# Optimization experiments

Measured on AMD Instinct MI355X. Metric: run time of the kernel, lower is better.

## Reference

```python
import jax, jax.numpy as jnp
import numpy as np
from jax import lax

NUM_IM, ROIS = 32, 128          # images per batch, proposals per image
NUM_CLASSES, EMBED, OBJ_DIM = 151, 200, 2048
HALF_H = 256                    # per-direction LSTM hidden; bi concat -> 512
BN_EPS = 1e-5


def _lstm_dir(xs, wih, whh, b):
    # xs: [T, B, Din] -> hidden states [T, B, H]
    pre = jnp.einsum('tbd,dh->tbh', xs, wih) + b  # precompute input proj
    H = whh.shape[0]
    h0 = jnp.zeros((xs.shape[1], H), xs.dtype)
    def step(carry, pt):
        h, c = carry
        g = pt + h @ whh
        i, f, gg, o = jnp.split(g, 4, axis=-1)
        c = jax.nn.sigmoid(f) * c + jax.nn.sigmoid(i) * jnp.tanh(gg)
        h = jax.nn.sigmoid(o) * jnp.tanh(c)
        return (h, c), h
    _, hs = lax.scan(step, (h0, h0), pre)
    return hs


def _bilstm(x, wih, whh, b):
    # x: [B, T, D] -> [B, T, 2*HALF_H]; wih/whh/b carry both directions on axis 0
    xs = jnp.swapaxes(x, 0, 1)
    fwd = _lstm_dir(xs, wih[0], whh[0], b[0])
    bwd = _lstm_dir(xs[::-1], wih[1], whh[1], b[1])[::-1]
    return jnp.swapaxes(jnp.concatenate([fwd, bwd], -1), 0, 1)


def _context(feats, conf, params):
    # sort_rois: per-image descending confidence order, run 2-layer bi(tree)LSTM,
    # then scatter back with the inverse permutation (as in _sort_by_score).
    D = feats.shape[-1]
    f = feats.reshape(NUM_IM, ROIS, D)
    perm = jnp.argsort(-conf.reshape(NUM_IM, ROIS), axis=1)
    xs = jnp.take_along_axis(f, perm[..., None], axis=1)
    wih0, whh0, b0, wih1, whh1, b1 = params
    h = _bilstm(xs, wih0, whh0, b0)
    h = _bilstm(h, wih1, whh1, b1)
    inv = jnp.argsort(perm, axis=1)
    h = jnp.take_along_axis(h, inv[..., None], axis=1)
    return h.reshape(NUM_IM * ROIS, -1)


def setup_inputs() -> dict:
    key = jax.random.key(0)
    ks = jax.random.split(key, 24)
    N = NUM_IM * ROIS
    obj_fmaps = jax.random.normal(ks[0], (N, OBJ_DIM), jnp.float32)
    obj_logits = jax.random.normal(ks[1], (N, NUM_CLASSES), jnp.float32)
    xy = jax.random.uniform(ks[2], (N, 2), jnp.float32) * 500.0
    wh = jax.random.uniform(ks[3], (N, 2), jnp.float32) * 100.0 + 1.0
    boxes = jnp.concatenate([xy, xy + wh], axis=1)  # valid x1y1x2y2
    im_inds = jnp.repeat(jnp.arange(NUM_IM, dtype=jnp.int64), ROIS)
    w = lambda k, s: (jax.random.normal(k, s, jnp.float32) * 0.02)
    H4 = 4 * HALF_H
    D_obj, D_edge = OBJ_DIM + EMBED + 128, EMBED + 2 * HALF_H + OBJ_DIM
    return {
        'obj_fmaps': obj_fmaps, 'obj_logits': obj_logits, 'boxes': boxes,
        'im_inds': im_inds,
        'obj_embed_w': w(ks[4], (NUM_CLASSES, EMBED)),
        'obj_embed2_w': w(ks[5], (NUM_CLASSES, EMBED)),
        'bn_gamma': jnp.ones((4,), jnp.float32), 'bn_beta': jnp.zeros((4,), jnp.float32),
        'bn_mean': jnp.zeros((4,), jnp.float32), 'bn_var': jnp.ones((4,), jnp.float32),
        'pos_w': w(ks[6], (4, 128)), 'pos_b': jnp.zeros((128,), jnp.float32),
        'obj_wih0': w(ks[7], (2, D_obj, H4)), 'obj_whh0': w(ks[8], (2, HALF_H, H4)),
        'obj_b0': jnp.zeros((2, H4), jnp.float32),
        'obj_wih1': w(ks[9], (2, 2 * HALF_H, H4)), 'obj_whh1': w(ks[10], (2, HALF_H, H4)),
        'obj_b1': jnp.zeros((2, H4), jnp.float32),
        'edge_wih0': w(ks[11], (2, D_edge, H4)), 'edge_whh0': w(ks[12], (2, HALF_H, H4)),
        'edge_b0': jnp.zeros((2, H4), jnp.float32),
        'edge_wih1': w(ks[13], (2, 2 * HALF_H, H4)), 'edge_whh1': w(ks[14], (2, HALF_H, H4)),
        'edge_b1': jnp.zeros((2, H4), jnp.float32),
        'dec_w': w(ks[15], (D_obj + 2 * HALF_H, NUM_CLASSES)),
        'dec_b': jnp.zeros((NUM_CLASSES,), jnp.float32),
    }


def reference(obj_fmaps, obj_logits, boxes, im_inds, obj_embed_w, obj_embed2_w,
              bn_gamma, bn_beta, bn_mean, bn_var, pos_w, pos_b,
              obj_wih0, obj_whh0, obj_b0, obj_wih1, obj_whh1, obj_b1,
              edge_wih0, edge_whh0, edge_b0, edge_wih1, edge_whh1, edge_b1,
              dec_w, dec_b):
    probs = jax.nn.softmax(obj_logits, axis=-1)
    obj_embed = probs @ obj_embed_w                      # soft class embedding
    x1, y1, x2, y2 = boxes[:, 0], boxes[:, 1], boxes[:, 2], boxes[:, 3]
    cs = jnp.stack([(x1 + x2) * 0.5, (y1 + y2) * 0.5, x2 - x1, y2 - y1], axis=-1)
    csn = (cs - bn_mean) * lax.rsqrt(bn_var + BN_EPS) * bn_gamma + bn_beta
    pos = jax.nn.relu(csn @ pos_w + pos_b)               # BN(4)+Linear(4,128)+ReLU
    feats = jnp.concatenate([obj_fmaps, obj_embed, pos], axis=-1)  # [N, 2376]
    conf = jnp.max(probs[:, 1:], axis=-1)                # confidence (non-bg)
    enc = _context(feats, conf, (obj_wih0, obj_whh0, obj_b0,
                                 obj_wih1, obj_whh1, obj_b1))       # [N, 512]
    dec_in = jnp.concatenate([feats, enc], axis=-1)      # pass_in_obj_feats_to_decoder
    obj_dists = dec_in @ dec_w + dec_b                   # [N, 151]
    obj_preds = jnp.argmax(obj_dists[:, 1:], axis=-1) + 1
    edge_in = jnp.concatenate([obj_embed2_w[obj_preds], enc, obj_fmaps], axis=-1)
    edge_ctx = _context(edge_in, conf, (edge_wih0, edge_whh0, edge_b0,
                                        edge_wih1, edge_whh1, edge_b1))  # [N, 512]
    return jnp.concatenate([obj_dists, edge_ctx], axis=-1)  # [N, 663]
```

## Files before the change

kernel.cpp:

```cpp
#include <hip/hip_runtime.h>
#include <hip/hip_bf16.h>
#include <hip/hip_fp16.h>

typedef unsigned short u16;
typedef unsigned char u8;
typedef unsigned int u32;
typedef short s16x8 __attribute__((ext_vector_type(8)));
typedef float f32x4 __attribute__((ext_vector_type(4)));
typedef int i32x4 __attribute__((ext_vector_type(4)));

#define FE_LD 2944
#define EDGE_LD 2816

static __device__ __forceinline__ int sdot4(u32 a, u32 b, int acc) {
  return __builtin_amdgcn_sdot4((int)a, (int)b, acc, false);
}
static __device__ __forceinline__ float fsig(float x) {
  return __builtin_amdgcn_rcpf(1.f + __expf(-x));
}
static __device__ __forceinline__ float ftanh(float x) {
  return 1.f - 2.f * __builtin_amdgcn_rcpf(1.f + __expf(2.f * x));
}
static __device__ __forceinline__ u16 f2bf_raw(float f) {
  return __builtin_bit_cast(u16, __float2bfloat16(f));
}

#define GLD_LDS16(gsrc, ldst) \
  __builtin_amdgcn_global_load_lds((const __attribute__((address_space(1))) void*)(gsrc), \
                                   (__attribute__((address_space(3))) void*)(ldst), 16, 0, 0)

static __device__ __forceinline__ void xcd_map(int gy, int* bx, int* by) {
  int lin = blockIdx.x;
  int q = gridDim.x >> 3;
  int wg = (lin & 7) * q + (lin >> 3);
  *bx = wg / gy; *by = wg % gy;
}

__global__ __launch_bounds__(256) void gemm_kernel(
    const u16* __restrict__ A, int lda,
    const u16* __restrict__ B, int ldb,
    int K, int N, int gy,
    float* __restrict__ outF, __hip_bfloat16* __restrict__ outB, int ldc,
    const float* __restrict__ bias)
{
  __shared__ __align__(16) u16 As[128*64];
  __shared__ __align__(16) u16 Bs[128*64];
  const int tid = threadIdx.x;
  const int w = tid >> 6, lane = tid & 63;
  const int wm = w >> 1, wn = w & 1;
  int bxi, byi; xcd_map(gy, &bxi, &byi);
  const long bm = (long)bxi * 128;
  const long bn = (long)byi * 128;
  f32x4 acc[4][4] = {};

  for (int k0 = 0; k0 < K; k0 += 64) {
    #pragma unroll
    for (int rr = 0; rr < 4; rr++) {
      int idx = rr * 256 + tid;
      int row = idx >> 3;
      int g   = idx & 7;
      int gs  = g ^ (row & 7);
      int ldst = (rr * 256 + (w << 6)) * 8;
      GLD_LDS16(A + (bm + row) * (long)lda + k0 + gs * 8, &As[ldst]);
      GLD_LDS16(B + (bn + row) * (long)ldb + k0 + gs * 8, &Bs[ldst]);
    }
    __syncthreads();
    #pragma unroll
    for (int kk = 0; kk < 2; kk++) {
      s16x8 af[4], bfr[4];
      #pragma unroll
      for (int i = 0; i < 4; i++) {
        int ra = wm * 64 + i * 16 + (lane & 15);
        int rb = wn * 64 + i * 16 + (lane & 15);
        int gg = kk * 4 + (lane >> 4);
        af[i]  = *(const s16x8*)&As[ra * 64 + ((gg ^ (ra & 7)) << 3)];
        bfr[i] = *(const s16x8*)&Bs[rb * 64 + ((gg ^ (rb & 7)) << 3)];
      }
      #pragma unroll
      for (int i = 0; i < 4; i++)
        #pragma unroll
        for (int j = 0; j < 4; j++)
          acc[i][j] = __builtin_amdgcn_mfma_f32_16x16x32_bf16(af[i], bfr[j], acc[i][j], 0, 0, 0);
    }
    __syncthreads();
  }

  #pragma unroll
  for (int i = 0; i < 4; i++)
    #pragma unroll
    for (int j = 0; j < 4; j++)
      #pragma unroll
      for (int v = 0; v < 4; v++) {
        long rr = bm + wm * 64 + i * 16 + (lane >> 4) * 4 + v;
        int  cc = (int)bn + wn * 64 + j * 16 + (lane & 15);
        if (cc < N) {
          float val = acc[i][j][v] + (bias ? bias[cc] : 0.f);
          if (outF) outF[rr * (long)ldc + cc] = val;
          else      outB[rr * (long)ldc + cc] = __float2bfloat16(val);
        }
      }
}

__global__ __launch_bounds__(256) void gemm_i8_kernel(
    const u8* __restrict__ A, int lda,
    const u8* __restrict__ B, int ldb,
    int K, int N, int gy,
    const float* __restrict__ asc, const float* __restrict__ bsc,
    __hip_bfloat16* __restrict__ outB, int ldc,
    const float* __restrict__ bias)
{
  __shared__ __align__(16) u8 As[128*128];
  __shared__ __align__(16) u8 Bs[128*128];
  const int tid = threadIdx.x;
  const int w = tid >> 6, lane = tid & 63;
  const int wm = w >> 1, wn = w & 1;
  int bxi, byi; xcd_map(gy, &bxi, &byi);
  const long bm = (long)bxi * 128;
  const long bn = (long)byi * 128;
  i32x4 acc[4][4] = {};

  for (int k0 = 0; k0 < K; k0 += 128) {
    #pragma unroll
    for (int rr = 0; rr < 4; rr++) {
      int idx = rr * 256 + tid;
      int row = idx >> 3;
      int g   = idx & 7;
      int gs  = g ^ (row & 7);
      int ldst = (rr * 256 + (w << 6)) * 16;
      GLD_LDS16(A + (bm + row) * (long)lda + k0 + gs * 16, &As[ldst]);
      GLD_LDS16(B + (bn + row) * (long)ldb + k0 + gs * 16, &Bs[ldst]);
    }
    __syncthreads();
    #pragma unroll
    for (int kk = 0; kk < 2; kk++) {
      i32x4 af[4], bfr[4];
      #pragma unroll
      for (int i = 0; i < 4; i++) {
        int ra = wm * 64 + i * 16 + (lane & 15);
        int rb = wn * 64 + i * 16 + (lane & 15);
        int gg = kk * 4 + (lane >> 4);
        af[i]  = __builtin_bit_cast(i32x4, *(const uint4*)&As[ra * 128 + ((gg ^ (ra & 7)) << 4)]);
        bfr[i] = __builtin_bit_cast(i32x4, *(const uint4*)&Bs[rb * 128 + ((gg ^ (rb & 7)) << 4)]);
      }
      #pragma unroll
      for (int i = 0; i < 4; i++)
        #pragma unroll
        for (int j = 0; j < 4; j++)
          acc[i][j] = __builtin_amdgcn_mfma_i32_16x16x64_i8(af[i], bfr[j], acc[i][j], 0, 0, 0);
    }
    __syncthreads();
  }

  #pragma unroll
  for (int i = 0; i < 4; i++)
    #pragma unroll
    for (int j = 0; j < 4; j++)
      #pragma unroll
      for (int v = 0; v < 4; v++) {
        long rr = bm + wm * 64 + i * 16 + (lane >> 4) * 4 + v;
        int  cc = (int)bn + wn * 64 + j * 16 + (lane & 15);
        if (cc < N) {
          float val = (float)acc[i][j][v] * asc[rr] * bsc[cc] + (bias ? bias[cc] : 0.f);
          outB[rr * (long)ldc + cc] = __float2bfloat16(val);
        }
      }
}

#define N_TROPS 9
struct SetupOps {
  const float* src[N_TROPS];
  __hip_bfloat16* dst[N_TROPS];
  int srcK[N_TROPS], srcN[N_TROPS], dstR[N_TROPS], dstC[N_TROPS];
  int split[N_TROPS], soff[N_TROPS];
  int tileBase[N_TROPS], tilesX[N_TROPS];
  int trEnd, pkEnd;
  const float* whh[4];
  u32* wreg[4]; u32* wlds[4]; float* wsc[4];
  const float* logits; const float* fmaps; const float* boxes;
  const float* bn_g; const float* bn_b; const float* bn_m; const float* bn_v;
  const float* pos_w; const float* pos_b; const float* embw;
  __hip_bfloat16* FE; u8* FEq; float* ascFE; float* conf;
};
__global__ __launch_bounds__(256) void setup_kernel(SetupOps ops)
{
  __shared__ __align__(16) float stage[2432];
  __shared__ float red[256];
  __shared__ float pf[151];
  const int bid = blockIdx.x, t = threadIdx.x;

  if (bid < ops.trEnd) {
    __shared__ float tile[64][65];
    int op = 0;
    #pragma unroll
    for (int i = 1; i < N_TROPS; i++) if (bid >= ops.tileBase[i]) op = i;
    const int local = bid - ops.tileBase[op];
    const int kt = (local % ops.tilesX[op]) * 64;
    const int nt = (local / ops.tilesX[op]) * 64;
    const float* src = ops.src[op];
    __hip_bfloat16* dst = ops.dst[op];
    const int srcK = ops.srcK[op], srcN = ops.srcN[op];
    const int dstR = ops.dstR[op], dstC = ops.dstC[op];
    const int split = ops.split[op], soff = ops.soff[op];
    {
      const int tx = t & 63, ty = t >> 6;
      #pragma unroll
      for (int i0 = 0; i0 < 16; i0++) {
        int i = i0 * 4 + ty;
        int k = kt + i;
        int srck = (k < split) ? (soff + k) : (k - split);
        int n = nt + tx;
        tile[i][tx] = (srck < srcK && n < srcN) ? src[(size_t)srck * srcN + n] : 0.f;
      }
    }
    __syncthreads();
    {
      const int cx = t & 31, iy = t >> 5;
      #pragma unroll
      for (int i0 = 0; i0 < 8; i0++) {
        int i = i0 * 8 + iy;
        int n = nt + i, k = kt + 2 * cx;
        if (n < dstR && k < dstC) {
          ushort2 h;
          h.x = f2bf_raw(tile[2 * cx][i]);
          h.y = f2bf_raw(tile[2 * cx + 1][i]);
          *(ushort2*)&dst[(size_t)n * dstC + k] = h;
        }
      }
    }
    return;
  }

  if (bid < ops.pkEnd) {
    const int local = bid - ops.trEnd;
    const int set = local >> 3;
    const int idx = (local & 7) * 256 + t;
    const float* whh = ops.whh[set];
    u32* wreg = ops.wreg[set];
    u32* wlds = ops.wlds[set];
    float* wsc = ops.wsc[set];
    const int d = idx >> 10, col = idx & 1023;
    const int c4 = col >> 8, j = col & 255;
    const float* s = whh + (size_t)d * 256 * 1024 + col;
    float mx = 0.f;
    for (int k = 0; k < 256; k++) mx = fmaxf(mx, fabsf(s[(size_t)k * 1024]));
    float inv = (mx > 0.f) ? 127.f / mx : 0.f;
    wsc[d * 1024 + col] = (mx > 0.f) ? mx / (127.f * 127.f) : 0.f;
    const int rc = (c4 < 2) ? 12 : 8;
    const int rb = (c4 == 0) ? 0 : (c4 == 1) ? 12 : (c4 == 2) ? 24 : 32;
    for (int kg = 0; kg < 4; kg++) {
      const int slot = kg * 256 + j;
      for (int w = 0; w < 16; w++) {
        u32 v = 0;
        #pragma unroll
        for (int b = 0; b < 4; b++) {
          int q = __float2int_rn(s[(size_t)(kg * 64 + 4 * w + b) * 1024] * inv);
          q = max(-127, min(127, q));
          v |= ((u32)(q & 0xff)) << (8 * b);
        }
        if (w < rc) {
          wreg[(size_t)(d * 40 + rb + w) * 1024 + slot] = v;
        } else {
          int qq, comp;
          if (c4 == 0)      { qq = 0; comp = w - 12; }
          else if (c4 == 1) { qq = 1; comp = w - 12; }
          else if (c4 == 2) { qq = 2 + ((w - 8) >> 2); comp = (w - 8) & 3; }
          else              { qq = 4 + ((w - 8) >> 2); comp = (w - 8) & 3; }
          wlds[((size_t)(d * 6 + qq) * 1024 + slot) * 4 + comp] = v;
        }
      }
    }
    return;
  }

  const int row = bid - ops.pkEnd;
  float v = (t < 151) ? ops.logits[(size_t)row * 151 + t] : -3.0e38f;
  red[t] = v; __syncthreads();
  for (int s = 128; s > 0; s >>= 1) { if (t < s) red[t] = fmaxf(red[t], red[t + s]); __syncthreads(); }
  float mx = red[0]; __syncthreads();
  float p = (t < 151) ? expf(v - mx) : 0.f;
  red[t] = p; __syncthreads();
  for (int s = 128; s > 0; s >>= 1) { if (t < s) red[t] += red[t + s]; __syncthreads(); }
  float sum = red[0]; __syncthreads();
  p = p / sum;
  if (t < 151) pf[t] = p;
  red[t] = (t >= 1 && t < 151) ? p : 0.f; __syncthreads();
  for (int s = 128; s > 0; s >>= 1) { if (t < s) red[t] = fmaxf(red[t], red[t + s]); __syncthreads(); }
  if (t == 0) ops.conf[row] = red[0];
  __syncthreads();

  __hip_bfloat16* FE = ops.FE + (size_t)row * FE_LD;
  {
    const float4* fm4 = (const float4*)(ops.fmaps + (size_t)row * 2048);
    for (int q4 = t; q4 < 512; q4 += 256) {
      float4 f = fm4[q4];
      *(float4*)&stage[q4 * 4] = f;
      ushort4 h;
      h.x = f2bf_raw(f.x); h.y = f2bf_raw(f.y); h.z = f2bf_raw(f.z); h.w = f2bf_raw(f.w);
      *(ushort4*)&FE[512 + q4 * 4] = h;
    }
  }
  if (t < 50) {
    const float4* ew4 = (const float4*)(ops.embw);
    float4 e = {0.f, 0.f, 0.f, 0.f};
    for (int k = 0; k < 151; k++) {
      float4 w = ew4[k * 50 + t];
      float pk = pf[k];
      e.x += pk * w.x; e.y += pk * w.y; e.z += pk * w.z; e.w += pk * w.w;
    }
    *(float4*)&stage[2048 + 4 * t] = e;
    ushort4 h;
    h.x = f2bf_raw(e.x); h.y = f2bf_raw(e.y); h.z = f2bf_raw(e.z); h.w = f2bf_raw(e.w);
    *(ushort4*)&FE[2560 + 4 * t] = h;
  }
  if (t < 128) {
    float x1 = ops.boxes[row * 4 + 0], y1 = ops.boxes[row * 4 + 1];
    float x2 = ops.boxes[row * 4 + 2], y2 = ops.boxes[row * 4 + 3];
    float cs[4] = { (x1 + x2) * 0.5f, (y1 + y2) * 0.5f, x2 - x1, y2 - y1 };
    float a = ops.pos_b[t];
    #pragma unroll
    for (int j = 0; j < 4; j++) {
      float cn = (cs[j] - ops.bn_m[j]) * rsqrtf(ops.bn_v[j] + 1e-5f) * ops.bn_g[j] + ops.bn_b[j];
      a += cn * ops.pos_w[j * 128 + t];
    }
    a = fmaxf(a, 0.f);
    stage[2248 + t] = a;
    FE[2760 + t] = __float2bfloat16(a);
  }
  if (t < 56) { stage[2376 + t] = 0.f; FE[2888 + t] = __float2bfloat16(0.f); }
  __syncthreads();

  float qm = 0.f;
  for (int c = t; c < 2432; c += 256) qm = fmaxf(qm, fabsf(stage[c]));
  red[t] = qm; __syncthreads();
  for (int s = 128; s > 0; s >>= 1) { if (t < s) red[t] = fmaxf(red[t], red[t + s]); __syncthreads(); }
  qm = red[0];
  float inv = (qm > 0.f) ? 127.f / qm : 0.f;
  if (t == 0) ops.ascFE[row] = (qm > 0.f) ? qm / 127.f : 0.f;
  u32* d32 = (u32*)(ops.FEq + (size_t)row * 2432);
  for (int wd = t; wd < 608; wd += 256) {
    u32 vv = 0;
    #pragma unroll
    for (int b = 0; b < 4; b++) {
      int q = __float2int_rn(stage[4 * wd + b] * inv);
      q = max(-127, min(127, q));
      vv |= ((u32)(q & 0xff)) << (8 * b);
    }
    d32[wd] = vv;
  }
}

__global__ __launch_bounds__(256) void quantw_sort_kernel(
    const u16* __restrict__ w0, u8* __restrict__ w0q, float* __restrict__ bsc0,
    const u16* __restrict__ w1, u8* __restrict__ w1q, float* __restrict__ bsc1,
    const float* __restrict__ conf, int* __restrict__ perm)
{
  const int bid = blockIdx.x, t = threadIdx.x;
  if (bid < 4096) {
    __shared__ float red[256];
    const int row = (bid < 2048) ? bid : (bid - 2048);
    const u16* src = (bid < 2048) ? w0 : w1;
    u8* dst = (bid < 2048) ? w0q : w1q;
    float* sc = (bid < 2048) ? bsc0 : bsc1;
    const int K = (bid < 2048) ? 2432 : 2816;
    const uint4* s4 = (const uint4*)(src + (size_t)row * K);
    const int K8 = K >> 3;
    float mx = 0.f;
    for (int c8 = t; c8 < K8; c8 += 256) {
      uint4 v = s4[c8];
      #pragma unroll
      for (int wi = 0; wi < 4; wi++) {
        u32 w = (wi == 0) ? v.x : (wi == 1) ? v.y : (wi == 2) ? v.z : v.w;
        mx = fmaxf(mx, fabsf(__builtin_bit_cast(float, w << 16)));
        mx = fmaxf(mx, fabsf(__builtin_bit_cast(float, w & 0xffff0000u)));
      }
    }
    red[t] = mx; __syncthreads();
    for (int st = 128; st > 0; st >>= 1) { if (t < st) red[t] = fmaxf(red[t], red[t + st]); __syncthreads(); }
    mx = red[0];
    float inv = (mx > 0.f) ? 127.f / mx : 0.f;
    if (t == 0) sc[row] = (mx > 0.f) ? mx / 127.f : 0.f;
    uint2* d64 = (uint2*)(dst + (size_t)row * K);
    for (int c8 = t; c8 < K8; c8 += 256) {
      uint4 v = s4[c8];
      u32 out[2] = {0, 0};
      #pragma unroll
      for (int wi = 0; wi < 4; wi++) {
        u32 w = (wi == 0) ? v.x : (wi == 1) ? v.y : (wi == 2) ? v.z : v.w;
        float f0 = __builtin_bit_cast(float, w << 16);
        float f1 = __builtin_bit_cast(float, w & 0xffff0000u);
        int q0 = max(-127, min(127, __float2int_rn(f0 * inv)));
        int q1 = max(-127, min(127, __float2int_rn(f1 * inv)));
        out[wi >> 1] |= ((u32)(q0 & 0xff)) << (16 * (wi & 1));
        out[wi >> 1] |= ((u32)(q1 & 0xff)) << (16 * (wi & 1) + 8);
      }
      d64[c8] = uint2{out[0], out[1]};
    }
    return;
  }
  {
    __shared__ float key[128];
    __shared__ int   idx[128];
    const int b = bid - 4096;
    if (t < 128) { key[t] = conf[b * 128 + t]; idx[t] = t; }
    __syncthreads();
    for (int k = 2; k <= 128; k <<= 1)
      for (int j = k >> 1; j > 0; j >>= 1) {
        if (t < 128) {
          int ixj = t ^ j;
          if (ixj > t) {
            bool up = (t & k) == 0;
            float ka = key[t], kb = key[ixj];
            int ia = idx[t], ib = idx[ixj];
            bool before = (ka > kb) || (ka == kb && ia < ib);
            if (before != up) { key[t] = kb; key[ixj] = ka; idx[t] = ib; idx[ixj] = ia; }
          }
        }
        __syncthreads();
      }
    if (t < 128) perm[b * 128 + t] = b * 128 + idx[t];
  }
}

__global__ __launch_bounds__(1024) void rec_kernel(
    const __hip_bfloat16* __restrict__ P,
    const int* __restrict__ perm,
    const u32* __restrict__ wreg_g,
    const uint4* __restrict__ wlds_g,
    const float* __restrict__ wsc_g,
    int gatherPerm, int outPerm,
    __hip_bfloat16* __restrict__ out_bf, int out_ld,
    float* __restrict__ out_f32, int f32_ld, int f32_off)
{
  __shared__ __align__(16) uint4 wt4[6 * 1024];
  __shared__ __align__(16) int4 part[256 * 5];
  __shared__ __align__(16) u32 hq[64];
  __shared__ int prow_lds[128];
  const int tid = threadIdx.x;
  const int kg = tid >> 8;
  const int img = blockIdx.x & 31, dir = blockIdx.x >> 5;

  u32 wv[40];
  {
    const u32* rp = wreg_g + (size_t)dir * 40960 + tid;
    #pragma unroll
    for (int i = 0; i < 40; i++) wv[i] = rp[(size_t)i * 1024];
  }
  #pragma unroll
  for (int i = 0; i < 40; i++) asm volatile("" : "+v"(wv[i]));
  {
    const uint4* lp = wlds_g + (size_t)dir * 6144 + tid;
    #pragma unroll
    for (int q = 0; q < 6; q++) wt4[q * 1024 + tid] = lp[(size_t)q * 1024];
  }
  if (tid < 128) prow_lds[tid] = perm[img * 128 + tid];
  if (tid < 64) hq[tid] = 0;

  float sc0 = 0.f, sc1 = 0.f, sc2 = 0.f, sc3 = 0.f, cst = 0.f;
  if (tid < 256) {
    const float* sp = wsc_g + dir * 1024 + tid;
    sc0 = sp[0]; sc1 = sp[256]; sc2 = sp[512]; sc3 = sp[768];
  }
  __syncthreads();

  const uint4* hq4 = (const uint4*)hq;

  int st = dir ? 127 : 0;
  float p0 = 0.f, p1 = 0.f, p2 = 0.f, p3 = 0.f;
  if (tid < 256) {
    int prow0 = gatherPerm ? prow_lds[st] : (img * 128 + st);
    const __hip_bfloat16* pp = P + (size_t)prow0 * 2048 + dir * 1024 + tid;
    p0 = __bfloat162float(pp[0]);   p1 = __bfloat162float(pp[256]);
    p2 = __bfloat162float(pp[512]); p3 = __bfloat162float(pp[768]);
  }

  for (int t = 0; t < 128; t++) {
    float n0 = 0.f, n1 = 0.f, n2 = 0.f, n3 = 0.f;
    if (tid < 256 && t < 127) {
      int stn = dir ? (126 - t) : (t + 1);
      int prn = gatherPerm ? prow_lds[stn] : (img * 128 + stn);
      const __hip_bfloat16* pp = P + (size_t)prn * 2048 + dir * 1024 + tid;
      n0 = __bfloat162float(pp[0]);   n1 = __bfloat162float(pp[256]);
      n2 = __bfloat162float(pp[512]); n3 = __bfloat162float(pp[768]);
    }

    int a0 = 0, a1 = 0, a2 = 0, a3 = 0;
    {
      uint4 hv = hq4[kg * 4 + 0];
      a0 = sdot4(hv.x, wv[0], a0);  a0 = sdot4(hv.y, wv[1], a0);
      a0 = sdot4(hv.z, wv[2], a0);  a0 = sdot4(hv.w, wv[3], a0);
      a1 = sdot4(hv.x, wv[12], a1); a1 = sdot4(hv.y, wv[13], a1);
      a1 = sdot4(hv.z, wv[14], a1); a1 = sdot4(hv.w, wv[15], a1);
      a2 = sdot4(hv.x, wv[24], a2); a2 = sdot4(hv.y, wv[25], a2);
      a2 = sdot4(hv.z, wv[26], a2); a2 = sdot4(hv.w, wv[27], a2);
      a3 = sdot4(hv.x, wv[32], a3); a3 = sdot4(hv.y, wv[33], a3);
      a3 = sdot4(hv.z, wv[34], a3); a3 = sdot4(hv.w, wv[35], a3);
    }
    {
      uint4 hv = hq4[kg * 4 + 1];
      a0 = sdot4(hv.x, wv[4], a0);  a0 = sdot4(hv.y, wv[5], a0);
      a0 = sdot4(hv.z, wv[6], a0);  a0 = sdot4(hv.w, wv[7], a0);
      a1 = sdot4(hv.x, wv[16], a1); a1 = sdot4(hv.y, wv[17], a1);
      a1 = sdot4(hv.z, wv[18], a1); a1 = sdot4(hv.w, wv[19], a1);
      a2 = sdot4(hv.x, wv[28], a2); a2 = sdot4(hv.y, wv[29], a2);
      a2 = sdot4(hv.z, wv[30], a2); a2 = sdot4(hv.w, wv[31], a2);
      a3 = sdot4(hv.x, wv[36], a3); a3 = sdot4(hv.y, wv[37], a3);
      a3 = sdot4(hv.z, wv[38], a3); a3 = sdot4(hv.w, wv[39], a3);
    }
    {
      uint4 hv = hq4[kg * 4 + 2];
      a0 = sdot4(hv.x, wv[8], a0);  a0 = sdot4(hv.y, wv[9], a0);
      a0 = sdot4(hv.z, wv[10], a0); a0 = sdot4(hv.w, wv[11], a0);
      a1 = sdot4(hv.x, wv[20], a1); a1 = sdot4(hv.y, wv[21], a1);
      a1 = sdot4(hv.z, wv[22], a1); a1 = sdot4(hv.w, wv[23], a1);
      uint4 wl = wt4[2 * 1024 + tid];
      a2 = sdot4(hv.x, wl.x, a2); a2 = sdot4(hv.y, wl.y, a2);
      a2 = sdot4(hv.z, wl.z, a2); a2 = sdot4(hv.w, wl.w, a2);
      wl = wt4[4 * 1024 + tid];
      a3 = sdot4(hv.x, wl.x, a3); a3 = sdot4(hv.y, wl.y, a3);
      a3 = sdot4(hv.z, wl.z, a3); a3 = sdot4(hv.w, wl.w, a3);
    }
    {
      uint4 hv = hq4[kg * 4 + 3];
      uint4 wl = wt4[0 * 1024 + tid];
      a0 = sdot4(hv.x, wl.x, a0); a0 = sdot4(hv.y, wl.y, a0);
      a0 = sdot4(hv.z, wl.z, a0); a0 = sdot4(hv.w, wl.w, a0);
      wl = wt4[1 * 1024 + tid];
      a1 = sdot4(hv.x, wl.x, a1); a1 = sdot4(hv.y, wl.y, a1);
      a1 = sdot4(hv.z, wl.z, a1); a1 = sdot4(hv.w, wl.w, a1);
      wl = wt4[3 * 1024 + tid];
      a2 = sdot4(hv.x, wl.x, a2); a2 = sdot4(hv.y, wl.y, a2);
      a2 = sdot4(hv.z, wl.z, a2); a2 = sdot4(hv.w, wl.w, a2);
      wl = wt4[5 * 1024 + tid];
      a3 = sdot4(hv.x, wl.x, a3); a3 = sdot4(hv.y, wl.y, a3);
      a3 = sdot4(hv.z, wl.z, a3); a3 = sdot4(hv.w, wl.w, a3);
    }

    part[(tid & 255) * 5 + kg] = int4{a0, a1, a2, a3};
    __syncthreads();

    if (tid < 256) {
      int4 q0 = part[tid * 5 + 0], q1 = part[tid * 5 + 1];
      int4 q2 = part[tid * 5 + 2], q3 = part[tid * 5 + 3];
      float gi = (float)(q0.x + q1.x + q2.x + q3.x) * sc0 + p0;
      float gf = (float)(q0.y + q1.y + q2.y + q3.y) * sc1 + p1;
      float gg = (float)(q0.z + q1.z + q2.z + q3.z) * sc2 + p2;
      float go = (float)(q0.w + q1.w + q2.w + q3.w) * sc3 + p3;
      float si = fsig(gi), sf = fsig(gf), so = fsig(go);
      cst = sf * cst + si * ftanh(gg);
      float h = so * ftanh(cst);
      int qi = __float2int_rn(h * 127.f);
      ((signed char*)hq)[tid] = (signed char)qi;
      const int orow = outPerm ? prow_lds[st] : (img * 128 + st);
      if (out_bf)  out_bf[(size_t)orow * out_ld + dir * 256 + tid] = __float2bfloat16(h);
      if (out_f32) out_f32[(size_t)orow * f32_ld + f32_off + dir * 256 + tid] = h;
    }
    __syncthreads();
    p0 = n0; p1 = n1; p2 = n2; p3 = n3;
    st = dir ? (st - 1) : (st + 1);
  }
}

__global__ __launch_bounds__(256) void argmax_edge_kernel(
    const float* __restrict__ dists,
    const float* __restrict__ embed2,
    const float* __restrict__ fmaps,
    const __hip_bfloat16* __restrict__ FE,
    u8* __restrict__ EDGEq, float* __restrict__ ascEDGE)
{
  __shared__ __align__(16) float stage[EDGE_LD];
  __shared__ float rv[256];
  __shared__ int   ri[256];
  const int row = blockIdx.x, t = threadIdx.x;

  float best = (t < 150) ? dists[(size_t)row * 663 + 1 + t] : -3.4e38f;
  int   bi   = (t < 150) ? (1 + t) : 1000;
  rv[t] = best; ri[t] = bi;
  __syncthreads();
  for (int s = 128; s > 0; s >>= 1) {
    if (t < s) {
      float ov = rv[t + s]; int oi = ri[t + s];
      if (ov > rv[t] || (ov == rv[t] && oi < ri[t])) { rv[t] = ov; ri[t] = oi; }
    }
    __syncthreads();
  }
  const int pr = ri[0];

  for (int c0 = t; c0 < 200; c0 += 256)
    stage[c0] = embed2[(size_t)pr * 200 + c0];
  if (t < 64) {
    const uint4* e4 = (const uint4*)(FE + (size_t)row * FE_LD);
    uint4 v = e4[t];
    #pragma unroll
    for (int wi = 0; wi < 4; wi++) {
      u32 w = (wi == 0) ? v.x : (wi == 1) ? v.y : (wi == 2) ? v.z : v.w;
      stage[200 + t * 8 + wi * 2]     = __builtin_bit_cast(float, w << 16);
      stage[200 + t * 8 + wi * 2 + 1] = __builtin_bit_cast(float, w & 0xffff0000u);
    }
  }
  {
    const float4* fm4 = (const float4*)(fmaps + (size_t)row * 2048);
    for (int c4 = t; c4 < 512; c4 += 256)
      *(float4*)&stage[712 + c4 * 4] = fm4[c4];
  }
  if (t < 56) stage[2760 + t] = 0.f;
  __syncthreads();

  float qm = 0.f;
  for (int c = t; c < EDGE_LD; c += 256) qm = fmaxf(qm, fabsf(stage[c]));
  rv[t] = qm; __syncthreads();
  for (int s = 128; s > 0; s >>= 1) { if (t < s) rv[t] = fmaxf(rv[t], rv[t + s]); __syncthreads(); }
  qm = rv[0];
  float inv = (qm > 0.f) ? 127.f / qm : 0.f;
  if (t == 0) ascEDGE[row] = (qm > 0.f) ? qm / 127.f : 0.f;
  uint2* d64 = (uint2*)(EDGEq + (size_t)row * EDGE_LD);
  for (int wd8 = t; wd8 < (EDGE_LD >> 3); wd8 += 256) {
    u32 out[2] = {0, 0};
    #pragma unroll
    for (int b = 0; b < 8; b++) {
      int q = __float2int_rn(stage[8 * wd8 + b] * inv);
      q = max(-127, min(127, q));
      out[b >> 2] |= ((u32)(q & 0xff)) << (8 * (b & 3));
    }
    d64[wd8] = uint2{out[0], out[1]};
  }
}

extern "C" void kernel_launch(void* const* d_in, const int* in_sizes, int n_in,
                              void* d_out, int out_size, void* d_ws, size_t ws_size,
                              hipStream_t stream)
{
  const float* obj_fmaps    = (const float*)d_in[0];
  const float* obj_logits   = (const float*)d_in[1];
  const float* boxes        = (const float*)d_in[2];
  const float* obj_embed_w  = (const float*)d_in[4];
  const float* obj_embed2_w = (const float*)d_in[5];
  const float* bn_g = (const float*)d_in[6];
  const float* bn_b = (const float*)d_in[7];
  const float* bn_m = (const float*)d_in[8];
  const float* bn_v = (const float*)d_in[9];
  const float* pos_w = (const float*)d_in[10];
  const float* pos_b = (const float*)d_in[11];
  const float* obj_wih0 = (const float*)d_in[12];
  const float* obj_whh0 = (const float*)d_in[13];
  const float* obj_b0   = (const float*)d_in[14];
  const float* obj_wih1 = (const float*)d_in[15];
  const float* obj_whh1 = (const float*)d_in[16];
  const float* obj_b1   = (const float*)d_in[17];
  const float* edge_wih0 = (const float*)d_in[18];
  const float* edge_whh0 = (const float*)d_in[19];
  const float* edge_b0   = (const float*)d_in[20];
  const float* edge_wih1 = (const float*)d_in[21];
  const float* edge_whh1 = (const float*)d_in[22];
  const float* edge_b1   = (const float*)d_in[23];
  const float* dec_w = (const float*)d_in[24];
  const float* dec_b = (const float*)d_in[25];
  float* out = (float*)d_out;

  char* ws = (char*)d_ws;
  auto alloc = [&](size_t bytes) -> char* {
    char* p = ws; ws += (bytes + 255) & ~(size_t)255; return p;
  };
  __hip_bfloat16* FE     = (__hip_bfloat16*)alloc(4096ull * FE_LD * 2);
  __hip_bfloat16* Pbuf   = (__hip_bfloat16*)alloc(4096ull * 2048 * 2);
  __hip_bfloat16* hseq   = (__hip_bfloat16*)alloc(4096ull * 512 * 2);
  __hip_bfloat16* wih0T  = (__hip_bfloat16*)alloc(2048ull * 2432 * 2);
  __hip_bfloat16* wih1T  = (__hip_bfloat16*)alloc(2048ull * 512 * 2);
  __hip_bfloat16* ewih0T = (__hip_bfloat16*)alloc(2048ull * 2816 * 2);
  __hip_bfloat16* ewih1T = (__hip_bfloat16*)alloc(2048ull * 512 * 2);
  __hip_bfloat16* decT   = (__hip_bfloat16*)alloc(256ull * 2944 * 2);
  u32* whh0pk  = (u32*)alloc(133120ull * 4);
  u32* whh1pk  = (u32*)alloc(133120ull * 4);
  u32* ewhh0pk = (u32*)alloc(133120ull * 4);
  u32* ewhh1pk = (u32*)alloc(133120ull * 4);
  u8*  FEq     = (u8*)alloc(4096ull * 2432);
  u8*  EDGEq   = (u8*)alloc(4096ull * 2816);
  u8*  wih0q   = (u8*)alloc(2048ull * 2432);
  u8*  ewih0q  = (u8*)alloc(2048ull * 2816);
  float* ascFE   = (float*)alloc(4096 * 4);
  float* ascEDGE = (float*)alloc(4096 * 4);
  float* bsc0    = (float*)alloc(2048 * 4);
  float* bsc1    = (float*)alloc(2048 * 4);
  int*   perm  = (int*)alloc(4096 * 4);
  float* conf  = (float*)alloc(4096 * 4);
  (void)in_sizes; (void)n_in; (void)out_size; (void)ws_size;

  SetupOps so{};
  int nt = 0, base = 0;
  auto addTr = [&](const float* src, __hip_bfloat16* dst, int srcK, int srcN,
                   int dstR, int dstC, int split, int soff) {
    so.src[nt] = src; so.dst[nt] = dst;
    so.srcK[nt] = srcK; so.srcN[nt] = srcN; so.dstR[nt] = dstR; so.dstC[nt] = dstC;
    so.split[nt] = split; so.soff[nt] = soff;
    int tx = (dstC + 63) / 64, ty = (dstR + 63) / 64;
    so.tileBase[nt] = base; so.tilesX[nt] = tx;
    base += tx * ty; nt++;
  };
  for (int d = 0; d < 2; d++) {
    addTr(obj_wih0 + (size_t)d * 2376 * 1024, wih0T + (size_t)d * 1024 * 2432, 2376, 1024, 1024, 2432, 0, 0);
    addTr(obj_wih1 + (size_t)d * 512 * 1024,  wih1T + (size_t)d * 1024 * 512,  512, 1024, 1024, 512, 0, 0);
    addTr(edge_wih0 + (size_t)d * 2760 * 1024, ewih0T + (size_t)d * 1024 * 2816, 2760, 1024, 1024, 2816, 0, 0);
    addTr(edge_wih1 + (size_t)d * 512 * 1024,  ewih1T + (size_t)d * 1024 * 512,  512, 1024, 1024, 512, 0, 0);
  }
  addTr(dec_w, decT, 2888, 151, 256, 2944, 512, 2376);
  so.trEnd = base;
  so.pkEnd = base + 32;
  const float* whhs[4] = {obj_whh0, obj_whh1, edge_whh0, edge_whh1};
  u32* pks[4] = {whh0pk, whh1pk, ewhh0pk, ewhh1pk};
  for (int i = 0; i < 4; i++) {
    so.whh[i] = whhs[i];
    so.wreg[i] = pks[i];
    so.wlds[i] = pks[i] + 81920;
    so.wsc[i]  = (float*)(pks[i] + 131072);
  }
  so.logits = obj_logits; so.fmaps = obj_fmaps; so.boxes = boxes;
  so.bn_g = bn_g; so.bn_b = bn_b; so.bn_m = bn_m; so.bn_v = bn_v;
  so.pos_w = pos_w; so.pos_b = pos_b; so.embw = obj_embed_w;
  so.FE = FE; so.FEq = FEq; so.ascFE = ascFE; so.conf = conf;
  setup_kernel<<<dim3(so.pkEnd + 4096), dim3(256), 0, stream>>>(so);

  quantw_sort_kernel<<<dim3(4128), dim3(256), 0, stream>>>(
      (const u16*)wih0T, wih0q, bsc0, (const u16*)ewih0T, ewih0q, bsc1, conf, perm);

  auto gemm = [&](const void* A, int lda, const void* B, int ldb, int K, int N,
                  float* oF, __hip_bfloat16* oB, int ldc, const float* bias) {
    int gy = (N + 127) / 128;
    gemm_kernel<<<dim3(32 * gy), dim3(256), 0, stream>>>(
        (const u16*)A, lda, (const u16*)B, ldb, K, N, gy, oF, oB, ldc, bias);
  };
  auto gemm_i8 = [&](const u8* A, int lda, const u8* B, int ldb, int K, int N,
                     const float* asc, const float* bsc,
                     __hip_bfloat16* oB, int ldc, const float* bias) {
    int gy = (N + 127) / 128;
    gemm_i8_kernel<<<dim3(32 * gy), dim3(256), 0, stream>>>(
        A, lda, B, ldb, K, N, gy, asc, bsc, oB, ldc, bias);
  };
  auto rec = [&](const __hip_bfloat16* P, const u32* wpk, int gat, int op,
                 __hip_bfloat16* ob, int old_, float* of, int fld, int foff) {
    rec_kernel<<<dim3(64), dim3(1024), 0, stream>>>(
        P, perm, wpk, (const uint4*)(wpk + 81920), (const float*)(wpk + 131072),
        gat, op, ob, old_, of, fld, foff);
  };

  gemm_i8(FEq, 2432, wih0q, 2432, 2432, 2048, ascFE, bsc0, Pbuf, 2048, obj_b0);
  rec(Pbuf, whh0pk, 1, 0, hseq, 512, nullptr, 0, 0);
  gemm(hseq, 512, wih1T, 512, 512, 2048, nullptr, Pbuf, 2048, obj_b1);
  rec(Pbuf, whh1pk, 0, 1, FE, FE_LD, nullptr, 0, 0);
  gemm(FE, FE_LD, decT, 2944, 2944, 151, out, nullptr, 663, dec_b);
  argmax_edge_kernel<<<dim3(4096), dim3(256), 0, stream>>>(
      out, obj_embed2_w, obj_fmaps, FE, EDGEq, ascEDGE);
  gemm_i8(EDGEq, 2816, ewih0q, 2816, 2816, 2048, ascEDGE, bsc1, Pbuf, 2048, edge_b0);
  rec(Pbuf, ewhh0pk, 1, 0, hseq, 512, nullptr, 0, 0);
  gemm(hseq, 512, ewih1T, 512, 512, 2048, nullptr, Pbuf, 2048, edge_b1);
  rec(Pbuf, ewhh1pk, 0, 1, nullptr, 0, out, 663, 151);
}
```

Before: 821.3 us.

## Quantize input weights directly from fp32 during transpose, skipping bf16 intermediate

The large layer-0 input-projection weights were previously transposed to bf16 and then re-read by a separate kernel that computed per-row scales and quantized them to int8. Now a first kernel computes partial per-column absolute maxima straight from the fp32 source. The transpose kernel then uses those maxima to write int8 output directly, and the bf16 intermediate buffers are dropped. This removes one full write and read of roughly 20 MB of bf16 weights, at the cost of a strided column-max pass over the fp32 weights. The scales are now derived from fp32 values rather than bf16-rounded ones, so the quantized weights can differ slightly.

```diff
diff --git a/kernel.cpp b/kernel.cpp
--- a/kernel.cpp
+++ b/kernel.cpp
@@ -166,14 +166,9 @@
       }
 }
 
-#define N_TROPS 9
-struct SetupOps {
-  const float* src[N_TROPS];
-  __hip_bfloat16* dst[N_TROPS];
-  int srcK[N_TROPS], srcN[N_TROPS], dstR[N_TROPS], dstC[N_TROPS];
-  int split[N_TROPS], soff[N_TROPS];
-  int tileBase[N_TROPS], tilesX[N_TROPS];
-  int trEnd, pkEnd;
+struct PrepA {
+  const float* objw; const float* edgew;
+  float* partial;
   const float* whh[4];
   u32* wreg[4]; u32* wlds[4]; float* wsc[4];
   const float* logits; const float* fmaps; const float* boxes;
@@ -181,57 +176,31 @@
   const float* pos_w; const float* pos_b; const float* embw;
   __hip_bfloat16* FE; u8* FEq; float* ascFE; float* conf;
 };
-__global__ __launch_bounds__(256) void setup_kernel(SetupOps ops)
+__global__ __launch_bounds__(256) void prepA_kernel(PrepA ops)
 {
   __shared__ __align__(16) float stage[2432];
   __shared__ float red[256];
   __shared__ float pf[151];
   const int bid = blockIdx.x, t = threadIdx.x;
 
-  if (bid < ops.trEnd) {
-    __shared__ float tile[64][65];
-    int op = 0;
-    #pragma unroll
-    for (int i = 1; i < N_TROPS; i++) if (bid >= ops.tileBase[i]) op = i;
-    const int local = bid - ops.tileBase[op];
-    const int kt = (local % ops.tilesX[op]) * 64;
-    const int nt = (local / ops.tilesX[op]) * 64;
-    const float* src = ops.src[op];
-    __hip_bfloat16* dst = ops.dst[op];
-    const int srcK = ops.srcK[op], srcN = ops.srcN[op];
-    const int dstR = ops.dstR[op], dstC = ops.dstC[op];
-    const int split = ops.split[op], soff = ops.soff[op];
-    {
-      const int tx = t & 63, ty = t >> 6;
-      #pragma unroll
-      for (int i0 = 0; i0 < 16; i0++) {
-        int i = i0 * 4 + ty;
-        int k = kt + i;
-        int srck = (k < split) ? (soff + k) : (k - split);
-        int n = nt + tx;
-        tile[i][tx] = (srck < srcK && n < srcN) ? src[(size_t)srck * srcN + n] : 0.f;
-      }
-    }
-    __syncthreads();
-    {
-      const int cx = t & 31, iy = t >> 5;
-      #pragma unroll
-      for (int i0 = 0; i0 < 8; i0++) {
-        int i = i0 * 8 + iy;
-        int n = nt + i, k = kt + 2 * cx;
-        if (n < dstR && k < dstC) {
-          ushort2 h;
-          h.x = f2bf_raw(tile[2 * cx][i]);
-          h.y = f2bf_raw(tile[2 * cx + 1][i]);
-          *(ushort2*)&dst[(size_t)n * dstC + k] = h;
-        }
-      }
-    }
+  if (bid < 128) {
+    const int set = bid >> 6;
+    const int b6 = bid & 63;
+    const int cb = b6 & 7, ks = b6 >> 3;
+    const int r = cb * 256 + t;
+    const int d = r >> 10, c = r & 1023;
+    const int K = set ? 2760 : 2376;
+    const int K8 = K / 8;
+    const float* src = (set ? ops.edgew : ops.objw) + (size_t)d * K * 1024 + c;
+    float m = 0.f;
+    for (int k = ks * K8; k < (ks + 1) * K8; k++)
+      m = fmaxf(m, fabsf(src[(size_t)k * 1024]));
+    ops.partial[(size_t)set * 16384 + ks * 2048 + r] = m;
     return;
   }
 
-  if (bid < ops.pkEnd) {
-    const int local = bid - ops.trEnd;
+  if (bid < 160) {
+    const int local = bid - 128;
     const int set = local >> 3;
     const int idx = (local & 7) * 256 + t;
     const float* whh = ops.whh[set];
@@ -272,7 +241,7 @@
     return;
   }
 
-  const int row = bid - ops.pkEnd;
+  const int row = bid - 160;
   float v = (t < 151) ? ops.logits[(size_t)row * 151 + t] : -3.0e38f;
   red[t] = v; __syncthreads();
   for (int s = 128; s > 0; s >>= 1) { if (t < s) red[t] = fmaxf(red[t], red[t + s]); __syncthreads(); }
@@ -349,59 +318,99 @@
   }
 }
 
-__global__ __launch_bounds__(256) void quantw_sort_kernel(
-    const u16* __restrict__ w0, u8* __restrict__ w0q, float* __restrict__ bsc0,
-    const u16* __restrict__ w1, u8* __restrict__ w1q, float* __restrict__ bsc1,
-    const float* __restrict__ conf, int* __restrict__ perm)
+#define N_OPS 9
+struct Setup2 {
+  const float* src[N_OPS];
+  void* dst[N_OPS];
+  const float* partial[N_OPS];
+  float* bscOut[N_OPS];
+  int rowBase[N_OPS];
+  int srcK[N_OPS], srcN[N_OPS], dstR[N_OPS], dstC[N_OPS];
+  int split[N_OPS], soff[N_OPS], isI8[N_OPS];
+  int tileBase[N_OPS], tilesX[N_OPS];
+  int trEnd;
+  const float* conf; int* perm;
+};
+__global__ __launch_bounds__(256) void setup2_kernel(Setup2 ops)
 {
   const int bid = blockIdx.x, t = threadIdx.x;
-  if (bid < 4096) {
-    __shared__ float red[256];
-    const int row = (bid < 2048) ? bid : (bid - 2048);
-    const u16* src = (bid < 2048) ? w0 : w1;
-    u8* dst = (bid < 2048) ? w0q : w1q;
-    float* sc = (bid < 2048) ? bsc0 : bsc1;
-    const int K = (bid < 2048) ? 2432 : 2816;
-    const uint4* s4 = (const uint4*)(src + (size_t)row * K);
-    const int K8 = K >> 3;
-    float mx = 0.f;
-    for (int c8 = t; c8 < K8; c8 += 256) {
-      uint4 v = s4[c8];
-      #pragma unroll
-      for (int wi = 0; wi < 4; wi++) {
-        u32 w = (wi == 0) ? v.x : (wi == 1) ? v.y : (wi == 2) ? v.z : v.w;
-        mx = fmaxf(mx, fabsf(__builtin_bit_cast(float, w << 16)));
-        mx = fmaxf(mx, fabsf(__builtin_bit_cast(float, w & 0xffff0000u)));
-      }
-    }
-    red[t] = mx; __syncthreads();
-    for (int st = 128; st > 0; st >>= 1) { if (t < st) red[t] = fmaxf(red[t], red[t + st]); __syncthreads(); }
-    mx = red[0];
-    float inv = (mx > 0.f) ? 127.f / mx : 0.f;
-    if (t == 0) sc[row] = (mx > 0.f) ? mx / 127.f : 0.f;
-    uint2* d64 = (uint2*)(dst + (size_t)row * K);
-    for (int c8 = t; c8 < K8; c8 += 256) {
-      uint4 v = s4[c8];
-      u32 out[2] = {0, 0};
-      #pragma unroll
-      for (int wi = 0; wi < 4; wi++) {
-        u32 w = (wi == 0) ? v.x : (wi == 1) ? v.y : (wi == 2) ? v.z : v.w;
-        float f0 = __builtin_bit_cast(float, w << 16);
-        float f1 = __builtin_bit_cast(float, w & 0xffff0000u);
-        int q0 = max(-127, min(127, __float2int_rn(f0 * inv)));
-        int q1 = max(-127, min(127, __float2int_rn(f1 * inv)));
-        out[wi >> 1] |= ((u32)(q0 & 0xff)) << (16 * (wi & 1));
-        out[wi >> 1] |= ((u32)(q1 & 0xff)) << (16 * (wi & 1) + 8);
-      }
-      d64[c8] = uint2{out[0], out[1]};
+  if (bid < ops.trEnd) {
+    __shared__ float tile[128 * 65];
+    __shared__ float invr[64];
+    int op = 0;
+    #pragma unroll
+    for (int i = 1; i < N_OPS; i++) if (bid >= ops.tileBase[i]) op = i;
+    const int local = bid - ops.tileBase[op];
+    const float* src = ops.src[op];
+    const int srcK = ops.srcK[op], srcN = ops.srcN[op];
+    const int dstC = ops.dstC[op];
+
+    if (ops.isI8[op]) {
+      const int kt = (local % ops.tilesX[op]) * 128;
+      const int nt = (local / ops.tilesX[op]) * 64;
+      u8* dst = (u8*)ops.dst[op];
+      const int tx = t & 63, ty = t >> 6;
+      #pragma unroll
+      for (int i0 = 0; i0 < 32; i0++) {
+        int k = i0 * 4 + ty;
+        int srck = kt + k;
+        tile[k * 65 + tx] = (srck < srcK) ? src[(size_t)srck * srcN + nt + tx] : 0.f;
+      }
+      if (t < 64) {
+        int g = ops.rowBase[op] + nt + t;
+        const float* pp = ops.partial[op];
+        float m = pp[g];
+        #pragma unroll
+        for (int s = 1; s < 8; s++) m = fmaxf(m, pp[s * 2048 + g]);
+        invr[t] = (m > 0.f) ? 127.f / m : 0.f;
+        if (kt == 0) ops.bscOut[op][g] = (m > 0.f) ? m / 127.f : 0.f;
+      }
+      __syncthreads();
+      const int k4 = t & 31, ng = t >> 5;
+      #pragma unroll
+      for (int pass = 0; pass < 8; pass++) {
+        int nl = pass * 8 + ng;
+        float inv = invr[nl];
+        u32 vv = 0;
+        #pragma unroll
+        for (int j = 0; j < 4; j++) {
+          int q = __float2int_rn(tile[(4 * k4 + j) * 65 + nl] * inv);
+          q = max(-127, min(127, q));
+          vv |= ((u32)(q & 0xff)) << (8 * j);
+        }
+        *(u32*)&dst[(size_t)(nt + nl) * dstC + kt + 4 * k4] = vv;
+      }
+    } else {
+      const int kt = (local % ops.tilesX[op]) * 64;
+      const int nt = (local / ops.tilesX[op]) * 64;
+      __hip_bfloat16* dst = (__hip_bfloat16*)ops.dst[op];
+      const int dstR = ops.dstR[op];
+      const int split = ops.split[op], soff = ops.soff[op];
+      const int tx = t & 63, ty = t >> 6;
+      #pragma unroll
+      for (int i0 = 0; i0 < 16; i0++) {
+        int i = i0 * 4 + ty;
+        int k = kt + i;
+        int srck = (k < split) ? (soff + k) : (k - split);
+        int n = nt + tx;
+        tile[i * 65 + tx] = (srck < srcK && n < srcN) ? src[(size_t)srck * srcN + n] : 0.f;
+      }
+      __syncthreads();
+      #pragma unroll
+      for (int i0 = 0; i0 < 16; i0++) {
+        int i = i0 * 4 + ty;
+        int n = nt + i, k = kt + tx;
+        if (n < dstR && k < dstC)
+          dst[(size_t)n * dstC + k] = __float2bfloat16(tile[tx * 65 + i]);
+      }
     }
     return;
   }
   {
     __shared__ float key[128];
     __shared__ int   idx[128];
-    const int b = bid - 4096;
-    if (t < 128) { key[t] = conf[b * 128 + t]; idx[t] = t; }
+    const int b = bid - ops.trEnd;
+    if (t < 128) { key[t] = ops.conf[b * 128 + t]; idx[t] = t; }
     __syncthreads();
     for (int k = 2; k <= 128; k <<= 1)
       for (int j = k >> 1; j > 0; j >>= 1) {
@@ -417,7 +426,7 @@
         }
         __syncthreads();
       }
-    if (t < 128) perm[b * 128 + t] = b * 128 + idx[t];
+    if (t < 128) ops.perm[b * 128 + t] = b * 128 + idx[t];
   }
 }
 
@@ -663,9 +672,7 @@
   __hip_bfloat16* FE     = (__hip_bfloat16*)alloc(4096ull * FE_LD * 2);
   __hip_bfloat16* Pbuf   = (__hip_bfloat16*)alloc(4096ull * 2048 * 2);
   __hip_bfloat16* hseq   = (__hip_bfloat16*)alloc(4096ull * 512 * 2);
-  __hip_bfloat16* wih0T  = (__hip_bfloat16*)alloc(2048ull * 2432 * 2);
   __hip_bfloat16* wih1T  = (__hip_bfloat16*)alloc(2048ull * 512 * 2);
-  __hip_bfloat16* ewih0T = (__hip_bfloat16*)alloc(2048ull * 2816 * 2);
   __hip_bfloat16* ewih1T = (__hip_bfloat16*)alloc(2048ull * 512 * 2);
   __hip_bfloat16* decT   = (__hip_bfloat16*)alloc(256ull * 2944 * 2);
   u32* whh0pk  = (u32*)alloc(133120ull * 4);
@@ -676,6 +683,7 @@
   u8*  EDGEq   = (u8*)alloc(4096ull * 2816);
   u8*  wih0q   = (u8*)alloc(2048ull * 2432);
   u8*  ewih0q  = (u8*)alloc(2048ull * 2816);
+  float* partial = (float*)alloc(2ull * 8 * 2048 * 4);
   float* ascFE   = (float*)alloc(4096 * 4);
   float* ascEDGE = (float*)alloc(4096 * 4);
   float* bsc0    = (float*)alloc(2048 * 4);
@@ -684,42 +692,61 @@
   float* conf  = (float*)alloc(4096 * 4);
   (void)in_sizes; (void)n_in; (void)out_size; (void)ws_size;
 
-  SetupOps so{};
-  int nt = 0, base = 0;
-  auto addTr = [&](const float* src, __hip_bfloat16* dst, int srcK, int srcN,
-                   int dstR, int dstC, int split, int soff) {
-    so.src[nt] = src; so.dst[nt] = dst;
-    so.srcK[nt] = srcK; so.srcN[nt] = srcN; so.dstR[nt] = dstR; so.dstC[nt] = dstC;
-    so.split[nt] = split; so.soff[nt] = soff;
-    int tx = (dstC + 63) / 64, ty = (dstR + 63) / 64;
-    so.tileBase[nt] = base; so.tilesX[nt] = tx;
-    base += tx * ty; nt++;
-  };
-  for (int d = 0; d < 2; d++) {
-    addTr(obj_wih0 + (size_t)d * 2376 * 1024, wih0T + (size_t)d * 1024 * 2432, 2376, 1024, 1024, 2432, 0, 0);
-    addTr(obj_wih1 + (size_t)d * 512 * 1024,  wih1T + (size_t)d * 1024 * 512,  512, 1024, 1024, 512, 0, 0);
-    addTr(edge_wih0 + (size_t)d * 2760 * 1024, ewih0T + (size_t)d * 1024 * 2816, 2760, 1024, 1024, 2816, 0, 0);
-    addTr(edge_wih1 + (size_t)d * 512 * 1024,  ewih1T + (size_t)d * 1024 * 512,  512, 1024, 1024, 512, 0, 0);
-  }
-  addTr(dec_w, decT, 2888, 151, 256, 2944, 512, 2376);
-  so.trEnd = base;
-  so.pkEnd = base + 32;
+  PrepA pa{};
+  pa.objw = obj_wih0; pa.edgew = edge_wih0; pa.partial = partial;
   const float* whhs[4] = {obj_whh0, obj_whh1, edge_whh0, edge_whh1};
   u32* pks[4] = {whh0pk, whh1pk, ewhh0pk, ewhh1pk};
   for (int i = 0; i < 4; i++) {
-    so.whh[i] = whhs[i];
-    so.wreg[i] = pks[i];
-    so.wlds[i] = pks[i] + 81920;
-    so.wsc[i]  = (float*)(pks[i] + 131072);
-  }
-  so.logits = obj_logits; so.fmaps = obj_fmaps; so.boxes = boxes;
-  so.bn_g = bn_g; so.bn_b = bn_b; so.bn_m = bn_m; so.bn_v = bn_v;
-  so.pos_w = pos_w; so.pos_b = pos_b; so.embw = obj_embed_w;
-  so.FE = FE; so.FEq = FEq; so.ascFE = ascFE; so.conf = conf;
-  setup_kernel<<<dim3(so.pkEnd + 4096), dim3(256), 0, stream>>>(so);
-
-  quantw_sort_kernel<<<dim3(4128), dim3(256), 0, stream>>>(
-      (const u16*)wih0T, wih0q, bsc0, (const u16*)ewih0T, ewih0q, bsc1, conf, perm);
+    pa.whh[i] = whhs[i];
+    pa.wreg[i] = pks[i];
+    pa.wlds[i] = pks[i] + 81920;
+    pa.wsc[i]  = (float*)(pks[i] + 131072);
+  }
+  pa.logits = obj_logits; pa.fmaps = obj_fmaps; pa.boxes = boxes;
+  pa.bn_g = bn_g; pa.bn_b = bn_b; pa.bn_m = bn_m; pa.bn_v = bn_v;
+  pa.pos_w = pos_w; pa.pos_b = pos_b; pa.embw = obj_embed_w;
+  pa.FE = FE; pa.FEq = FEq; pa.ascFE = ascFE; pa.conf = conf;
+  prepA_kernel<<<dim3(160 + 4096), dim3(256), 0, stream>>>(pa);
+
+  Setup2 s2{};
+  int nOps = 0, base = 0;
+  auto addI8 = [&](const float* src, u8* dst, const float* part, float* bsc,
+                   int rowBase, int srcK, int dstC) {
+    int i = nOps++;
+    s2.src[i] = src; s2.dst[i] = dst; s2.partial[i] = part; s2.bscOut[i] = bsc;
+    s2.rowBase[i] = rowBase;
+    s2.srcK[i] = srcK; s2.srcN[i] = 1024; s2.dstR[i] = 1024; s2.dstC[i] = dstC;
+    s2.split[i] = 0; s2.soff[i] = 0; s2.isI8[i] = 1;
+    s2.tileBase[i] = base; s2.tilesX[i] = dstC / 128;
+    base += (dstC / 128) * (1024 / 64);
+  };
+  auto addBf = [&](const float* src, __hip_bfloat16* dst, int srcK, int srcN,
+                   int dstR, int dstC, int split, int soff) {
+    int i = nOps++;
+    s2.src[i] = src; s2.dst[i] = dst; s2.partial[i] = nullptr; s2.bscOut[i] = nullptr;
+    s2.rowBase[i] = 0;
+    s2.srcK[i] = srcK; s2.srcN[i] = srcN; s2.dstR[i] = dstR; s2.dstC[i] = dstC;
+    s2.split[i] = split; s2.soff[i] = soff; s2.isI8[i] = 0;
+    int tx = (dstC + 63) / 64, ty = (dstR + 63) / 64;
+    s2.tileBase[i] = base; s2.tilesX[i] = tx;
+    base += tx * ty;
+  };
+  for (int d = 0; d < 2; d++)
+    addI8(obj_wih0 + (size_t)d * 2376 * 1024, wih0q + (size_t)d * 1024 * 2432,
+          partial, bsc0, d * 1024, 2376, 2432);
+  for (int d = 0; d < 2; d++)
+    addI8(edge_wih0 + (size_t)d * 2760 * 1024, ewih0q + (size_t)d * 1024 * 2816,
+          partial + 16384, bsc1, d * 1024, 2760, 2816);
+  for (int d = 0; d < 2; d++)
+    addBf(obj_wih1 + (size_t)d * 512 * 1024, wih1T + (size_t)d * 1024 * 512,
+          512, 1024, 1024, 512, 0, 0);
+  for (int d = 0; d < 2; d++)
+    addBf(edge_wih1 + (size_t)d * 512 * 1024, ewih1T + (size_t)d * 1024 * 512,
+          512, 1024, 1024, 512, 0, 0);
+  addBf(dec_w, decT, 2888, 151, 256, 2944, 512, 2376);
+  s2.trEnd = base;
+  s2.conf = conf; s2.perm = perm;
+  setup2_kernel<<<dim3(base + 32), dim3(256), 0, stream>>>(s2);
 
   auto gemm = [&](const void* A, int lda, const void* B, int ldb, int K, int N,
                   float* oF, __hip_bfloat16* oB, int ldc, const float* bias) {
```

New measurement: 824.4 us. No clear change (+0.4%).
